# Kernel optimization log

Hardware: AMD Instinct MI355X
Metric: run time of the kernel (lower is better)

## Reference

```python
import jax, jax.numpy as jnp
import numpy as np

D_MODEL = 512
INF = 1e9
TEMP = np.sqrt(D_MODEL).astype(np.float32)


def setup_inputs() -> dict:
    key = jax.random.key(0)
    kq, kk, kv, km = jax.random.split(key, 4)
    B, L, D = 64, 1024, 64  # B = batch*heads
    q = jax.random.normal(kq, (B, L, D), dtype=jnp.float32)
    k = jax.random.normal(kk, (B, L, D), dtype=jnp.float32)
    v = jax.random.normal(kv, (B, L, D), dtype=jnp.float32)
    attn_mask = jax.random.randint(km, (B, L, L), 0, 2).astype(jnp.bool_)
    return {"q": q, "k": k, "v": v, "attn_mask": attn_mask}


def reference(q, k, v, attn_mask):
    # scores: [b, len_q, len_k]
    attn = jnp.einsum('bqd,bkd->bqk', q, k) / TEMP
    attn = jnp.where(attn_mask, -INF, attn)
    attn = jax.nn.softmax(attn, axis=2)
    # dropout p=0.0 -> identity
    out = jnp.einsum('bqk,bkd->bqd', attn, v)
    return out
```

## Files before the change

kernel.cpp:

```cpp
#include <hip/hip_runtime.h>
#include <hip/hip_bf16.h>


typedef __attribute__((ext_vector_type(4))) float f32x4;
typedef __attribute__((ext_vector_type(8))) short bf16x8;
typedef __attribute__((ext_vector_type(4))) short short4v;

constexpr int B_ = 64;
constexpr int L_ = 1024;
constexpr int D_ = 64;
constexpr int QBLK = 64;
constexpr int KV = 64;
constexpr int NKV = L_ / KV;
constexpr int PAD = 8;
constexpr int STR = KV + PAD;
constexpr int STRB = 72;
constexpr float INV_TEMP = 0.04419417382415922f;
constexpr float NEG = -1e9f;

__device__ inline short f2bf(float f) {
  __hip_bfloat16 h = __float2bfloat16(f);
  short s; __builtin_memcpy(&s, &h, 2);
  return s;
}

__global__ __launch_bounds__(256) void attn_fwd(
    const float* __restrict__ Q, const float* __restrict__ K,
    const float* __restrict__ V, const int* __restrict__ M,
    float* __restrict__ O)
{
  __shared__ short k_lds[KV][STR];
  __shared__ short vt_lds[D_][STR];
  __shared__ short p_lds[4][16][STR];
  __shared__ unsigned char m_lds[QBLK][STRB];

  const int qt   = blockIdx.x;
  const int b    = blockIdx.y;
  const int tid  = threadIdx.x;
  const int w    = tid >> 6;
  const int lane = tid & 63;
  const int g    = lane >> 4;
  const int c    = lane & 15;

  const int q0 = qt * QBLK;

  bf16x8 qf[2];
  {
    const int qrow = q0 + w * 16 + c;
    const float* qp = Q + ((size_t)b * L_ + qrow) * D_ + g * 8;
#pragma unroll
    for (int ks = 0; ks < 2; ++ks) {
      f32x4 x0 = *(const f32x4*)(qp + ks * 32);
      f32x4 x1 = *(const f32x4*)(qp + ks * 32 + 4);
      bf16x8 t;
      t[0] = f2bf(x0[0]); t[1] = f2bf(x0[1]); t[2] = f2bf(x0[2]); t[3] = f2bf(x0[3]);
      t[4] = f2bf(x1[0]); t[5] = f2bf(x1[1]); t[6] = f2bf(x1[2]); t[7] = f2bf(x1[3]);
      qf[ks] = t;
    }
  }

  const float* Kb = K + (size_t)b * L_ * D_;
  const float* Vb = V + (size_t)b * L_ * D_;
  const int*   Mb = M + (size_t)b * L_ * L_ + (size_t)q0 * L_;

  f32x4 kreg[4], vreg[4];
  int4  mreg[4];

  auto stage_load = [&](int t) {
    const float* ksrc = Kb + (size_t)(t * KV) * D_;
    const float* vsrc = Vb + (size_t)(t * KV) * D_;
    const int*   msrc = Mb + t * KV;
#pragma unroll
    for (int i = 0; i < 4; ++i) {
      const int idx = tid + i * 256;
      const int key = idx >> 4;
      const int d4  = (idx & 15) * 4;
      kreg[i] = *(const f32x4*)(ksrc + (size_t)idx * 4);
      vreg[i] = *(const f32x4*)(vsrc + (size_t)idx * 4);
      mreg[i] = *(const int4*)(msrc + (size_t)key * L_ + d4);
    }
  };

  auto stage_write = [&]() {
    const int rot = (tid & 15) >> 1;
#pragma unroll
    for (int i = 0; i < 4; ++i) {
      const int idx = tid + i * 256;
      const int key = idx >> 4;
      const int d4  = (idx & 15) * 4;
      f32x4 kx = kreg[i];
      short4v ks4 = { f2bf(kx[0]), f2bf(kx[1]), f2bf(kx[2]), f2bf(kx[3]) };
      *(short4v*)&k_lds[key][d4] = ks4;
      f32x4 vx = vreg[i];
#pragma unroll
      for (int j = 0; j < 4; ++j) {
        const int jj = (j + rot) & 3;
        vt_lds[d4 + jj][key] = f2bf(vx[jj]);
      }
      int4 mm = mreg[i];
      unsigned int packed = (unsigned int)(mm.x != 0)
                          | ((unsigned int)(mm.y != 0) << 8)
                          | ((unsigned int)(mm.z != 0) << 16)
                          | ((unsigned int)(mm.w != 0) << 24);
      *(unsigned int*)&m_lds[key][d4] = packed;
    }
  };

  f32x4 acc[4];
#pragma unroll
  for (int i = 0; i < 4; ++i) acc[i] = (f32x4){0.f, 0.f, 0.f, 0.f};
  float m_run[4] = {-INFINITY, -INFINITY, -INFINITY, -INFINITY};
  float l_run[4] = {0.f, 0.f, 0.f, 0.f};

  stage_load(0);
  stage_write();
  __syncthreads();

  for (int t = 0; t < NKV; ++t) {
    const bool has_next = (t + 1 < NKV);
    if (has_next) stage_load(t + 1);

    f32x4 sc[4];
#pragma unroll
    for (int f = 0; f < 4; ++f) {
      f32x4 a = (f32x4){0.f, 0.f, 0.f, 0.f};
#pragma unroll
      for (int ks = 0; ks < 2; ++ks) {
        bf16x8 kf = *(const bf16x8*)&k_lds[f * 16 + c][ks * 32 + g * 8];
        a = __builtin_amdgcn_mfma_f32_16x16x32_bf16(qf[ks], kf, a, 0, 0, 0);
      }
      sc[f] = a;
    }

#pragma unroll
    for (int f = 0; f < 4; ++f) {
#pragma unroll
      for (int r = 0; r < 4; ++r) {
        unsigned char mm = m_lds[w * 16 + g * 4 + r][f * 16 + c];
        sc[f][r] = mm ? NEG : sc[f][r] * INV_TEMP;
      }
    }

    float m_new[4], alpha[4];
#pragma unroll
    for (int r = 0; r < 4; ++r) {
      float x = fmaxf(fmaxf(sc[0][r], sc[1][r]), fmaxf(sc[2][r], sc[3][r]));
#pragma unroll
      for (int sh = 1; sh < 16; sh <<= 1) x = fmaxf(x, __shfl_xor(x, sh, 64));
      m_new[r] = fmaxf(m_run[r], x);
      alpha[r] = __expf(m_run[r] - m_new[r]);
    }
#pragma unroll
    for (int f = 0; f < 4; ++f)
#pragma unroll
      for (int r = 0; r < 4; ++r)
        sc[f][r] = __expf(sc[f][r] - m_new[r]);
#pragma unroll
    for (int r = 0; r < 4; ++r) {
      float s = (sc[0][r] + sc[1][r]) + (sc[2][r] + sc[3][r]);
#pragma unroll
      for (int sh = 1; sh < 16; sh <<= 1) s += __shfl_xor(s, sh, 64);
      l_run[r] = l_run[r] * alpha[r] + s;
      m_run[r] = m_new[r];
    }
#pragma unroll
    for (int fd = 0; fd < 4; ++fd)
#pragma unroll
      for (int r = 0; r < 4; ++r) acc[fd][r] *= alpha[r];

#pragma unroll
    for (int f = 0; f < 4; ++f)
#pragma unroll
      for (int r = 0; r < 4; ++r)
        p_lds[w][g * 4 + r][f * 16 + c] = f2bf(sc[f][r]);

#pragma unroll
    for (int ks = 0; ks < 2; ++ks) {
      bf16x8 pa = *(const bf16x8*)&p_lds[w][c][ks * 32 + g * 8];
#pragma unroll
      for (int fd = 0; fd < 4; ++fd) {
        bf16x8 vb = *(const bf16x8*)&vt_lds[fd * 16 + c][ks * 32 + g * 8];
        acc[fd] = __builtin_amdgcn_mfma_f32_16x16x32_bf16(pa, vb, acc[fd], 0, 0, 0);
      }
    }

    __syncthreads();
    if (has_next) stage_write();
    __syncthreads();
  }

  float inv_l[4];
#pragma unroll
  for (int r = 0; r < 4; ++r) inv_l[r] = 1.0f / l_run[r];
  float* orow = O + ((size_t)b * L_ + q0 + w * 16 + g * 4) * D_;
#pragma unroll
  for (int fd = 0; fd < 4; ++fd)
#pragma unroll
    for (int r = 0; r < 4; ++r)
      orow[(size_t)r * D_ + fd * 16 + c] = acc[fd][r] * inv_l[r];
}

extern "C" void kernel_launch(void* const* d_in, const int* in_sizes, int n_in,
                              void* d_out, int out_size, void* d_ws, size_t ws_size,
                              hipStream_t stream) {
  const float* q = (const float*)d_in[0];
  const float* k = (const float*)d_in[1];
  const float* v = (const float*)d_in[2];
  const int* m = (const int*)d_in[3];
  float* o = (float*)d_out;
  dim3 grid(L_ / QBLK, B_);
  attn_fwd<<<grid, 256, 0, stream>>>(q, k, v, m, o);
}
```

Baseline: 104.8 us.

## Transpose score MFMA layout, vectorize mask/P LDS access and V transpose stores

The Q·K MFMA operands are swapped so each lane holds scores for a single query row across keys. Row max and sum reductions then need only two cross-lane shuffles instead of four per row, and per-row running stats collapse to one scalar per lane, redistributed with __shfl when rescaling the accumulator. Mask reads from LDS become one 32-bit load per fragment and P is written as packed short4. V is loaded in a 4x4 register tile so the transpose into LDS uses short4 stores instead of scalar bf16 stores. The trade-off is less contiguous global V loads and extra shuffles for alpha and 1/l.

```diff
diff --git a/kernel.cpp b/kernel.cpp
--- a/kernel.cpp
+++ b/kernel.cpp
@@ -12,8 +12,7 @@
 constexpr int QBLK = 64;
 constexpr int KV = 64;
 constexpr int NKV = L_ / KV;
-constexpr int PAD = 8;
-constexpr int STR = KV + PAD;
+constexpr int STR = 72;
 constexpr int STRB = 72;
 constexpr float INV_TEMP = 0.04419417382415922f;
 constexpr float NEG = -1e9f;
@@ -46,8 +45,7 @@
 
   bf16x8 qf[2];
   {
-    const int qrow = q0 + w * 16 + c;
-    const float* qp = Q + ((size_t)b * L_ + qrow) * D_ + g * 8;
+    const float* qp = Q + ((size_t)b * L_ + q0 + w * 16 + c) * D_ + g * 8;
 #pragma unroll
     for (int ks = 0; ks < 2; ++ks) {
       f32x4 x0 = *(const f32x4*)(qp + ks * 32);
@@ -65,6 +63,8 @@
 
   f32x4 kreg[4], vreg[4];
   int4  mreg[4];
+  const int vkey4 = (tid & 15) * 4;
+  const int vd4   = (tid >> 4) * 4;
 
   auto stage_load = [&](int t) {
     const float* ksrc = Kb + (size_t)(t * KV) * D_;
@@ -73,44 +73,41 @@
 #pragma unroll
     for (int i = 0; i < 4; ++i) {
       const int idx = tid + i * 256;
-      const int key = idx >> 4;
+      const int row = idx >> 4;
       const int d4  = (idx & 15) * 4;
       kreg[i] = *(const f32x4*)(ksrc + (size_t)idx * 4);
-      vreg[i] = *(const f32x4*)(vsrc + (size_t)idx * 4);
-      mreg[i] = *(const int4*)(msrc + (size_t)key * L_ + d4);
+      mreg[i] = *(const int4*)(msrc + (size_t)row * L_ + d4);
+      vreg[i] = *(const f32x4*)(vsrc + (size_t)(vkey4 + i) * D_ + vd4);
     }
   };
 
   auto stage_write = [&]() {
-    const int rot = (tid & 15) >> 1;
 #pragma unroll
     for (int i = 0; i < 4; ++i) {
       const int idx = tid + i * 256;
-      const int key = idx >> 4;
+      const int row = idx >> 4;
       const int d4  = (idx & 15) * 4;
       f32x4 kx = kreg[i];
       short4v ks4 = { f2bf(kx[0]), f2bf(kx[1]), f2bf(kx[2]), f2bf(kx[3]) };
-      *(short4v*)&k_lds[key][d4] = ks4;
-      f32x4 vx = vreg[i];
-#pragma unroll
-      for (int j = 0; j < 4; ++j) {
-        const int jj = (j + rot) & 3;
-        vt_lds[d4 + jj][key] = f2bf(vx[jj]);
-      }
+      *(short4v*)&k_lds[row][d4] = ks4;
       int4 mm = mreg[i];
       unsigned int packed = (unsigned int)(mm.x != 0)
                           | ((unsigned int)(mm.y != 0) << 8)
                           | ((unsigned int)(mm.z != 0) << 16)
                           | ((unsigned int)(mm.w != 0) << 24);
-      *(unsigned int*)&m_lds[key][d4] = packed;
+      *(unsigned int*)&m_lds[row][d4] = packed;
+      const int jj = (i + (tid >> 4)) & 3;
+      short4v vt4 = { f2bf(vreg[0][jj]), f2bf(vreg[1][jj]),
+                      f2bf(vreg[2][jj]), f2bf(vreg[3][jj]) };
+      *(short4v*)&vt_lds[vd4 + jj][vkey4] = vt4;
     }
   };
 
   f32x4 acc[4];
 #pragma unroll
   for (int i = 0; i < 4; ++i) acc[i] = (f32x4){0.f, 0.f, 0.f, 0.f};
-  float m_run[4] = {-INFINITY, -INFINITY, -INFINITY, -INFINITY};
-  float l_run[4] = {0.f, 0.f, 0.f, 0.f};
+  float m_run = -INFINITY;
+  float l_run = 0.f;
 
   stage_load(0);
   stage_write();
@@ -127,52 +124,57 @@
 #pragma unroll
       for (int ks = 0; ks < 2; ++ks) {
         bf16x8 kf = *(const bf16x8*)&k_lds[f * 16 + c][ks * 32 + g * 8];
-        a = __builtin_amdgcn_mfma_f32_16x16x32_bf16(qf[ks], kf, a, 0, 0, 0);
+        a = __builtin_amdgcn_mfma_f32_16x16x32_bf16(kf, qf[ks], a, 0, 0, 0);
       }
       sc[f] = a;
     }
 
+    const unsigned char* mrow = &m_lds[w * 16 + c][0];
 #pragma unroll
     for (int f = 0; f < 4; ++f) {
+      const unsigned int mm4 = *(const unsigned int*)(mrow + f * 16 + 4 * g);
 #pragma unroll
       for (int r = 0; r < 4; ++r) {
-        unsigned char mm = m_lds[w * 16 + g * 4 + r][f * 16 + c];
-        sc[f][r] = mm ? NEG : sc[f][r] * INV_TEMP;
-      }
-    }
-
-    float m_new[4], alpha[4];
-#pragma unroll
-    for (int r = 0; r < 4; ++r) {
-      float x = fmaxf(fmaxf(sc[0][r], sc[1][r]), fmaxf(sc[2][r], sc[3][r]));
-#pragma unroll
-      for (int sh = 1; sh < 16; sh <<= 1) x = fmaxf(x, __shfl_xor(x, sh, 64));
-      m_new[r] = fmaxf(m_run[r], x);
-      alpha[r] = __expf(m_run[r] - m_new[r]);
-    }
+        sc[f][r] = ((mm4 >> (8 * r)) & 0xffu) ? NEG : sc[f][r] * INV_TEMP;
+      }
+    }
+
+    float x = -INFINITY;
 #pragma unroll
     for (int f = 0; f < 4; ++f)
 #pragma unroll
-      for (int r = 0; r < 4; ++r)
-        sc[f][r] = __expf(sc[f][r] - m_new[r]);
-#pragma unroll
-    for (int r = 0; r < 4; ++r) {
-      float s = (sc[0][r] + sc[1][r]) + (sc[2][r] + sc[3][r]);
-#pragma unroll
-      for (int sh = 1; sh < 16; sh <<= 1) s += __shfl_xor(s, sh, 64);
-      l_run[r] = l_run[r] * alpha[r] + s;
-      m_run[r] = m_new[r];
-    }
+      for (int r = 0; r < 4; ++r) x = fmaxf(x, sc[f][r]);
+    x = fmaxf(x, __shfl_xor(x, 16, 64));
+    x = fmaxf(x, __shfl_xor(x, 32, 64));
+    const float m_new = fmaxf(m_run, x);
+    const float alpha = __expf(m_run - m_new);
+    float s = 0.f;
+#pragma unroll
+    for (int f = 0; f < 4; ++f)
+#pragma unroll
+      for (int r = 0; r < 4; ++r) {
+        sc[f][r] = __expf(sc[f][r] - m_new);
+        s += sc[f][r];
+      }
+    s += __shfl_xor(s, 16, 64);
+    s += __shfl_xor(s, 32, 64);
+    l_run = l_run * alpha + s;
+    m_run = m_new;
+
+    float ar[4];
+#pragma unroll
+    for (int r = 0; r < 4; ++r)
+      ar[r] = __shfl(alpha, (lane & 48) | (g * 4 + r), 64);
 #pragma unroll
     for (int fd = 0; fd < 4; ++fd)
 #pragma unroll
-      for (int r = 0; r < 4; ++r) acc[fd][r] *= alpha[r];
-
-#pragma unroll
-    for (int f = 0; f < 4; ++f)
-#pragma unroll
-      for (int r = 0; r < 4; ++r)
-        p_lds[w][g * 4 + r][f * 16 + c] = f2bf(sc[f][r]);
+      for (int r = 0; r < 4; ++r) acc[fd][r] *= ar[r];
+
+#pragma unroll
+    for (int f = 0; f < 4; ++f) {
+      short4v pk = { f2bf(sc[f][0]), f2bf(sc[f][1]), f2bf(sc[f][2]), f2bf(sc[f][3]) };
+      *(short4v*)&p_lds[w][c][f * 16 + 4 * g] = pk;
+    }
 
 #pragma unroll
     for (int ks = 0; ks < 2; ++ks) {
@@ -189,15 +191,17 @@
     __syncthreads();
   }
 
-  float inv_l[4];
-#pragma unroll
-  for (int r = 0; r < 4; ++r) inv_l[r] = 1.0f / l_run[r];
+  const float li = 1.0f / l_run;
+  float lr[4];
+#pragma unroll
+  for (int r = 0; r < 4; ++r)
+    lr[r] = __shfl(li, (lane & 48) | (g * 4 + r), 64);
   float* orow = O + ((size_t)b * L_ + q0 + w * 16 + g * 4) * D_;
 #pragma unroll
   for (int fd = 0; fd < 4; ++fd)
 #pragma unroll
     for (int r = 0; r < 4; ++r)
-      orow[(size_t)r * D_ + fd * 16 + c] = acc[fd][r] * inv_l[r];
+      orow[(size_t)r * D_ + fd * 16 + c] = acc[fd][r] * lr[r];
 }
 
 extern "C" void kernel_launch(void* const* d_in, const int* in_sizes, int n_in,
```

Result: slower. 108.9 us (+3.9%).
